# Optimization experiments

Hardware: AMD Instinct MI355X
Metric: run time of the kernel (lower is better)

## Reference

```python
import jax, jax.numpy as jnp
import numpy as np

WH, WW = 7, 7
N_TOK = WH * WW


def _buffers():
    # relative_coords_table: [1, 2*WH-1, 2*WW-1, 2], Swin-V2 log-spaced coords
    ch = np.arange(-(WH - 1), WH, dtype=np.float32)
    cw = np.arange(-(WW - 1), WW, dtype=np.float32)
    t = np.stack(np.meshgrid(ch, cw, indexing='ij'), axis=-1)[None]
    t[..., 0] /= (WH - 1)
    t[..., 1] /= (WW - 1)
    t *= 8.0
    t = np.sign(t) * np.log2(np.abs(t) + 1.0) / np.log2(8.0)
    # relative_position_index: [N, N]
    coords = np.stack(np.meshgrid(np.arange(WH), np.arange(WW), indexing='ij'))
    cf = coords.reshape(2, -1)
    rc = (cf[:, :, None] - cf[:, None, :]).transpose(1, 2, 0).astype(np.int32)
    rc[..., 0] += WH - 1
    rc[..., 1] += WW - 1
    rc[..., 0] *= 2 * WW - 1
    idx = rc.sum(-1)
    return jnp.asarray(t, jnp.float32), jnp.asarray(idx, jnp.int32)


def setup_inputs() -> dict:
    key = jax.random.key(0)
    ks = jax.random.split(key, 10)
    C, H = 384, 12
    B_, nW = 2048, 64
    rel_table, rel_index = _buffers()
    s = 0.02
    return {
        'x': jax.random.normal(ks[0], (B_, N_TOK, C), jnp.float32),
        'mask': jax.random.normal(ks[1], (nW, N_TOK, N_TOK), jnp.float32),
        'qkv_w': jax.random.normal(ks[2], (3 * C, C), jnp.float32) * s,
        'q_bias': jnp.zeros((C,), jnp.float32),
        'v_bias': jnp.zeros((C,), jnp.float32),
        'logit_scale': jnp.full((H, 1, 1), np.log(10.0), jnp.float32),
        'cpb_w1': jax.random.normal(ks[3], (512, 2), jnp.float32) * s,
        'cpb_b1': jnp.zeros((512,), jnp.float32),
        'cpb_w2': jax.random.normal(ks[4], (H, 512), jnp.float32) * s,
        'proj_w': jax.random.normal(ks[5], (C, C), jnp.float32) * s,
        'proj_b': jnp.zeros((C,), jnp.float32),
        'rel_table': rel_table,
        'rel_index': rel_index,
    }


def reference(x, mask, qkv_w, q_bias, v_bias, logit_scale, cpb_w1, cpb_b1,
              cpb_w2, proj_w, proj_b, rel_table, rel_index):
    B_, N, C = x.shape
    H = logit_scale.shape[0]
    Dh = C // H
    nW = mask.shape[0]
    # qkv projection with q/v bias, zero bias for k
    qkv_bias = jnp.concatenate([q_bias, jnp.zeros_like(v_bias), v_bias])
    qkv = x @ qkv_w.T + qkv_bias                       # [B, N, 3C]
    qkv = qkv.reshape(B_, N, 3, H, Dh).transpose(2, 0, 3, 1, 4)
    q, k, v = qkv[0], qkv[1], qkv[2]                    # [B, H, N, Dh]
    # per-head clamped logit scale
    ls = jnp.exp(jnp.minimum(logit_scale, np.log(1.0 / 0.01)))  # [H,1,1]
    # continuous relative position bias via small MLP
    tbl = jax.nn.relu(rel_table @ cpb_w1.T + cpb_b1) @ cpb_w2.T  # [1,13,13,H]
    tbl = tbl.reshape(-1, H)
    rpb = tbl[rel_index.reshape(-1)].reshape(N, N, H).transpose(2, 0, 1)
    rpb = 16.0 * jax.nn.sigmoid(rpb)                    # [H, N, N]
    # cosine attention (kernel uses norm + 1e-6 in denominator)
    qn = q / (jnp.sqrt(jnp.sum(q * q, -1, keepdims=True)) + 1e-6)
    kn = k / (jnp.sqrt(jnp.sum(k * k, -1, keepdims=True)) + 1e-6)
    attn = jnp.einsum('bhnd,bhmd->bhnm', qn, kn) * ls[None]
    attn = attn + rpb[None]
    # shift mask: window index w = batch_index % nW
    attn = attn.reshape(B_ // nW, nW, H, N, N) + mask[None, :, None]
    attn = attn.reshape(B_, H, N, N)
    # stable softmax with kernel's +1e-6 in denominator
    m = jnp.max(attn, -1, keepdims=True)
    e = jnp.exp(attn - m)
    p = e / (jnp.sum(e, -1, keepdims=True) + 1e-6)
    out = jnp.einsum('bhnm,bhmd->bhnd', p, v)           # [B, H, N, Dh]
    out = out.transpose(0, 2, 1, 3).reshape(B_, N, C)
    return out @ proj_w.T + proj_b
```

## Files before the change

### kernel.cpp

```cpp
#include <hip/hip_runtime.h>
#include <hip/hip_bf16.h>

typedef __attribute__((ext_vector_type(8))) short bf16x8;
typedef __attribute__((ext_vector_type(4))) float f32x4;
typedef __attribute__((ext_vector_type(16))) float f32x16;
typedef __attribute__((ext_vector_type(8))) unsigned short u16x8;
typedef unsigned short ushort_t;

#define DEVFN static __device__ __forceinline__

DEVFN ushort_t f2bf(float f) {
  unsigned int u = __builtin_bit_cast(unsigned int, f);
  u += 0x7FFFu + ((u >> 16) & 1u);
  return (ushort_t)(u >> 16);
}

DEVFN unsigned int cvtpk_bf16(float lo, float hi) {
  unsigned int r;
  asm("v_cvt_pk_bf16_f32 %0, %1, %2" : "=v"(r) : "v"(lo), "v"(hi));
  return r;
}

DEVFN void gload_lds16(const ushort_t* g, ushort_t* l) {
  __builtin_amdgcn_global_load_lds(
      (const __attribute__((address_space(1))) void*)g,
      (__attribute__((address_space(3))) void*)l, 16, 0, 0);
}

#define WAIT_VM(n) do { asm volatile("s_waitcnt vmcnt(" #n ")" ::: "memory"); \
                        __builtin_amdgcn_sched_barrier(0); } while (0)
#define WAIT_LGKM0 do { asm volatile("s_waitcnt lgkmcnt(0)" ::: "memory"); \
                        __builtin_amdgcn_sched_barrier(0); } while (0)
#define RAW_BAR __builtin_amdgcn_s_barrier()

DEVFN int xcd_swz(int bid, int nwg) {
  int q = nwg >> 3, r = nwg & 7;
  int xcd = bid & 7, u = bid >> 3;
  return (xcd < r ? xcd * (q + 1) : r * (q + 1) + (xcd - r) * q) + u;
}

__global__ void k_prep_w(const float* __restrict__ qkv_w, const float* __restrict__ proj_w,
                         const float* __restrict__ q_bias, const float* __restrict__ v_bias,
                         ushort_t* __restrict__ qkv_wb, ushort_t* __restrict__ proj_wb,
                         float* __restrict__ qkv_bias) {
  int gid = blockIdx.x * blockDim.x + threadIdx.x;
  int stride = gridDim.x * blockDim.x;
  for (int i = gid; i < 1152 * 384; i += stride) qkv_wb[i] = f2bf(qkv_w[i]);
  for (int i = gid; i < 384 * 384; i += stride) proj_wb[i] = f2bf(proj_w[i]);
  for (int i = gid; i < 1152; i += stride)
    qkv_bias[i] = (i < 384) ? q_bias[i] : ((i < 768) ? 0.f : v_bias[i - 768]);
}

__global__ void k_xb(const float* __restrict__ x, ushort_t* __restrict__ xb, long n4) {
  long gid = (long)blockIdx.x * blockDim.x + threadIdx.x;
  long stride = (long)gridDim.x * blockDim.x;
  for (long i = gid; i < n4; i += stride) {
    float4 v = reinterpret_cast<const float4*>(x)[i];
    unsigned long long pk = (unsigned long long)f2bf(v.x) |
                            ((unsigned long long)f2bf(v.y) << 16) |
                            ((unsigned long long)f2bf(v.z) << 32) |
                            ((unsigned long long)f2bf(v.w) << 48);
    reinterpret_cast<unsigned long long*>(xb)[i] = pk;
  }
}

__global__ void k_prep_cpb(const float* __restrict__ rel_table, const float* __restrict__ cpb_w1,
                           const float* __restrict__ cpb_b1, const float* __restrict__ cpb_w2,
                           const float* __restrict__ logit_scale,
                           float* __restrict__ tbl, float* __restrict__ ls) {
  int lane = threadIdx.x;
  if (blockIdx.x == 169) {
    if (lane < 12) ls[lane] = __expf(fminf(logit_scale[lane], 4.605170185988092f));
    return;
  }
  int row = blockIdx.x;
  float t0 = rel_table[row * 2 + 0], t1 = rel_table[row * 2 + 1];
  float acc[12];
#pragma unroll
  for (int h = 0; h < 12; h++) acc[h] = 0.f;
  for (int j = lane; j < 512; j += 64) {
    float hj = fmaxf(cpb_w1[j * 2] * t0 + cpb_w1[j * 2 + 1] * t1 + cpb_b1[j], 0.f);
#pragma unroll
    for (int h = 0; h < 12; h++) acc[h] += cpb_w2[h * 512 + j] * hj;
  }
#pragma unroll
  for (int h = 0; h < 12; h++) {
    float v = acc[h];
    v += __shfl_xor(v, 1);  v += __shfl_xor(v, 2);  v += __shfl_xor(v, 4);
    v += __shfl_xor(v, 8);  v += __shfl_xor(v, 16); v += __shfl_xor(v, 32);
    if (lane == 0) tbl[row * 12 + h] = v;
  }
}

__global__ void k_prep_comb(const float* __restrict__ tbl, const int* __restrict__ rel_index,
                            const float* __restrict__ mask, float* __restrict__ comb) {
  int gid = blockIdx.x * blockDim.x + threadIdx.x;
  if (gid >= 64 * 12 * 2401) return;
  int ij = gid % 2401;
  int h = (gid / 2401) % 12;
  int w = gid / (2401 * 12);
  float t = tbl[rel_index[ij] * 12 + h];
  comb[gid] = 16.f / (1.f + __expf(-t)) + mask[w * 2401 + ij];
}

__global__ void __launch_bounds__(256, 2) k_qkv(const ushort_t* __restrict__ xb,
                                                const ushort_t* __restrict__ wb,
                                                const float* __restrict__ bias,
                                                const float* __restrict__ lsb,
                                                ushort_t* __restrict__ qkvn, int nmb) {
  __shared__ __align__(16) ushort_t As[2][128][64];
  __shared__ __align__(16) ushort_t Bs[2][128][64];
  const int tid = threadIdx.x;
  const int lane = tid & 63, wid = tid >> 6;
  const int wm = wid >> 1, wn = wid & 1;
  const int l15 = lane & 15, g = lane >> 4;
  const int t = xcd_swz(blockIdx.x, nmb * 9);
  const int m0 = (t / 9) * 128, n0 = (t % 9) * 128;
  f32x4 acc[4][4] = {};

  const int rb_ = (wid << 3) + (lane >> 3);
  const int cg_ = (lane & 7) ^ (rb_ & 7);
  const size_t so_ = (size_t)rb_ * 384 + cg_ * 8;
  const int lo_ = wid * 512;
  const ushort_t* gA = xb + (size_t)m0 * 384 + so_;
  const ushort_t* gB = wb + (size_t)n0 * 384 + so_;

#define QKV_STAGE(buf, kk)                                                   \
  {                                                                          \
    _Pragma("unroll")                                                        \
    for (int it = 0; it < 4; it++) {                                         \
      gload_lds16(gA + (kk) * 64 + (size_t)it * 12288,                       \
                  &As[buf][0][0] + lo_ + it * 2048);                         \
      gload_lds16(gB + (kk) * 64 + (size_t)it * 12288,                       \
                  &Bs[buf][0][0] + lo_ + it * 2048);                         \
    }                                                                        \
  }

#define QKV_COMPUTE(buf)                                                     \
  {                                                                          \
    _Pragma("unroll")                                                        \
    for (int ks = 0; ks < 64; ks += 32) {                                    \
      const int cxor = (ks >> 3) + g;                                        \
      bf16x8 a[4], b[4];                                                     \
      _Pragma("unroll")                                                      \
      for (int mi = 0; mi < 4; mi++) {                                       \
        int row = wm * 64 + mi * 16 + l15;                                   \
        a[mi] = *reinterpret_cast<const bf16x8*>(                            \
            &As[buf][row][(cxor ^ (row & 7)) * 8]);                          \
      }                                                                      \
      _Pragma("unroll")                                                      \
      for (int ni = 0; ni < 4; ni++) {                                       \
        int row = wn * 64 + ni * 16 + l15;                                   \
        b[ni] = *reinterpret_cast<const bf16x8*>(                            \
            &Bs[buf][row][(cxor ^ (row & 7)) * 8]);                          \
      }                                                                      \
      _Pragma("unroll")                                                      \
      for (int mi = 0; mi < 4; mi++)                                         \
        _Pragma("unroll")                                                    \
        for (int ni = 0; ni < 4; ni++)                                       \
          acc[mi][ni] = __builtin_amdgcn_mfma_f32_16x16x32_bf16(             \
              a[mi], b[ni], acc[mi][ni], 0, 0, 0);                           \
    }                                                                        \
  }

  QKV_STAGE(0, 0);
  QKV_STAGE(1, 1);
  WAIT_VM(8); RAW_BAR;
  QKV_COMPUTE(0); WAIT_LGKM0; RAW_BAR;
  QKV_STAGE(0, 2); WAIT_VM(8); RAW_BAR;
  QKV_COMPUTE(1); WAIT_LGKM0; RAW_BAR;
  QKV_STAGE(1, 3); WAIT_VM(8); RAW_BAR;
  QKV_COMPUTE(0); WAIT_LGKM0; RAW_BAR;
  QKV_STAGE(0, 4); WAIT_VM(8); RAW_BAR;
  QKV_COMPUTE(1); WAIT_LGKM0; RAW_BAR;
  QKV_STAGE(1, 5); WAIT_VM(8); RAW_BAR;
  QKV_COMPUTE(0); WAIT_LGKM0; RAW_BAR;
  WAIT_VM(0); RAW_BAR;
  QKV_COMPUTE(1);
#undef QKV_STAGE
#undef QKV_COMPUTE

  const int colbase = n0 + wn * 64;
  const int which = colbase / 384;
  const float scl0 = (which == 0) ? lsb[(colbase >> 5)] : 1.f;
  const float scl1 = (which == 0) ? lsb[(colbase >> 5) + 1] : 1.f;
  float bs[4];
#pragma unroll
  for (int ni = 0; ni < 4; ni++) bs[ni] = bias[colbase + ni * 16 + l15];
#pragma unroll
  for (int mi = 0; mi < 4; mi++) {
#pragma unroll
    for (int r = 0; r < 4; r++) {
      float v[4];
#pragma unroll
      for (int ni = 0; ni < 4; ni++) v[ni] = acc[mi][ni][r] + bs[ni];
      if (which < 2) {
        float ss0 = v[0] * v[0] + v[1] * v[1];
        float ss1 = v[2] * v[2] + v[3] * v[3];
        ss0 += __shfl_xor(ss0, 1); ss1 += __shfl_xor(ss1, 1);
        ss0 += __shfl_xor(ss0, 2); ss1 += __shfl_xor(ss1, 2);
        ss0 += __shfl_xor(ss0, 4); ss1 += __shfl_xor(ss1, 4);
        ss0 += __shfl_xor(ss0, 8); ss1 += __shfl_xor(ss1, 8);
        float rn0 = scl0 / (sqrtf(ss0) + 1e-6f);
        float rn1 = scl1 / (sqrtf(ss1) + 1e-6f);
        v[0] *= rn0; v[1] *= rn0; v[2] *= rn1; v[3] *= rn1;
      }
      int row = m0 + wm * 64 + mi * 16 + g * 4 + r;
      size_t base = (size_t)row * 1152 + colbase + l15;
#pragma unroll
      for (int ni = 0; ni < 4; ni++) qkvn[base + ni * 16] = f2bf(v[ni]);
    }
  }
}

__global__ void __launch_bounds__(256, 4) k_attn(const ushort_t* __restrict__ qkvn,
                                                 const float* __restrict__ comb,
                                                 ushort_t* __restrict__ attn,
                                                 int win_base, int nk) {
  __shared__ float comb_s[2401];
  __shared__ __align__(16) ushort_t Vt[4][32][72];
  const int tid = threadIdx.x;
  const int lane = tid & 63, wv = tid >> 6;
  const int l31 = lane & 31, hi = lane >> 5;
  const int h = blockIdx.y;
  const int wloc = blockIdx.x & 63;
  const int k = (blockIdx.x >> 6) * 4 + wv;
  const bool active = k < nk;
  const int w_abs = (win_base + wloc) & 63;

  {
    const float* ct = comb + ((size_t)w_abs * 12 + h) * 2401;
    for (int i = tid; i < 2401; i += 256) comb_s[i] = ct[i];
  }

  const size_t rowbase = (size_t)(wloc + 64 * k) * 49;

  if (active) {
#pragma unroll
    for (int pass = 0; pass < 4; pass++) {
      int t = pass * 16 + (lane >> 2);
      int d0 = (lane & 3) * 8;
      u16x8 v = {};
      if (t < 49)
        v = *reinterpret_cast<const u16x8*>(&qkvn[(rowbase + t) * 1152 + 768 + h * 32 + d0]);
#pragma unroll
      for (int j = 0; j < 8; j++) Vt[wv][d0 + j][t] = v[j];
    }
  }
  __syncthreads();
  if (!active) return;

  bf16x8 qf[2][2], kf[2][2];
#pragma unroll
  for (int b = 0; b < 2; b++) {
    int t = b * 32 + l31; if (t > 48) t = 48;
    size_t rb = (rowbase + t) * 1152 + h * 32 + hi * 8;
#pragma unroll
    for (int ks = 0; ks < 2; ks++) {
      qf[b][ks] = *reinterpret_cast<const bf16x8*>(&qkvn[rb + ks * 16]);
      kf[b][ks] = *reinterpret_cast<const bf16x8*>(&qkvn[rb + 384 + ks * 16]);
    }
  }
  f32x16 S[2][2] = {};
#pragma unroll
  for (int a = 0; a < 2; a++)
#pragma unroll
    for (int b = 0; b < 2; b++) {
      S[a][b] = __builtin_amdgcn_mfma_f32_32x32x16_bf16(kf[a][0], qf[b][0], S[a][b], 0, 0, 0);
      S[a][b] = __builtin_amdgcn_mfma_f32_32x32x16_bf16(kf[a][1], qf[b][1], S[a][b], 0, 0, 0);
    }

#pragma unroll
  for (int b = 0; b < 2; b++) {
    const int qt = b * 32 + l31;
    const int qi = qt > 48 ? 48 : qt;
    const float* crow_p = &comb_s[qi * 49];
    float m = -3.0e38f;
#pragma unroll
    for (int a = 0; a < 2; a++)
#pragma unroll
      for (int r = 0; r < 16; r++) {
        int kt = a * 32 + (r & 3) + 8 * (r >> 2) + 4 * hi;
        float v = (kt < 49) ? (S[a][b][r] + crow_p[kt]) : -3.0e38f;
        S[a][b][r] = v;
        m = fmaxf(m, v);
      }
    m = fmaxf(m, __shfl_xor(m, 32));
    float s = 0.f;
#pragma unroll
    for (int a = 0; a < 2; a++)
#pragma unroll
      for (int r = 0; r < 16; r++) {
        float e = __expf(S[a][b][r] - m);
        S[a][b][r] = e;
        s += e;
      }
    s += __shfl_xor(s, 32);
    const float inv = 1.f / (s + 1e-6f);
    unsigned int pkk[2][4][2];
#pragma unroll
    for (int a = 0; a < 2; a++)
#pragma unroll
      for (int c = 0; c < 4; c++) {
        pkk[a][c][0] = cvtpk_bf16(S[a][b][c * 4 + 0] * inv, S[a][b][c * 4 + 1] * inv);
        pkk[a][c][1] = cvtpk_bf16(S[a][b][c * 4 + 2] * inv, S[a][b][c * 4 + 3] * inv);
      }
    f32x16 O = {};
#pragma unroll
    for (int a = 0; a < 2; a++)
#pragma unroll
      for (int ks = 0; ks < 2; ks++) {
        unsigned int s0 = hi ? pkk[a][2 * ks][0] : pkk[a][2 * ks + 1][0];
        unsigned int s1 = hi ? pkk[a][2 * ks][1] : pkk[a][2 * ks + 1][1];
        unsigned int r0 = __shfl_xor(s0, 32);
        unsigned int r1 = __shfl_xor(s1, 32);
        unsigned int w0 = hi ? r0 : pkk[a][2 * ks][0];
        unsigned int w1 = hi ? r1 : pkk[a][2 * ks][1];
        unsigned int w2 = hi ? pkk[a][2 * ks + 1][0] : r0;
        unsigned int w3 = hi ? pkk[a][2 * ks + 1][1] : r1;
        uint4 wq = {w0, w1, w2, w3};
        bf16x8 pa = __builtin_bit_cast(bf16x8, wq);
        bf16x8 vb = *reinterpret_cast<const bf16x8*>(&Vt[wv][l31][a * 32 + ks * 16 + hi * 8]);
        O = __builtin_amdgcn_mfma_f32_32x32x16_bf16(pa, vb, O, 0, 0, 0);
      }
#pragma unroll
    for (int r = 0; r < 16; r++) {
      int qrow = b * 32 + (r & 3) + 8 * (r >> 2) + 4 * hi;
      if (qrow < 49)
        attn[(rowbase + qrow) * 384 + h * 32 + l31] = f2bf(O[r]);
    }
  }
}

__global__ void __launch_bounds__(256, 2) k_proj(const ushort_t* __restrict__ a,
                                                 const ushort_t* __restrict__ wb,
                                                 const float* __restrict__ pbias,
                                                 float* __restrict__ out, int nmb) {
  __shared__ __align__(16) ushort_t As[2][128][64];
  __shared__ __align__(16) ushort_t Bs[2][128][64];
  const int tid = threadIdx.x;
  const int lane = tid & 63, wid = tid >> 6;
  const int wm = wid >> 1, wn = wid & 1;
  const int l15 = lane & 15, g = lane >> 4;
  const int t = xcd_swz(blockIdx.x, nmb * 3);
  const int m0 = (t / 3) * 128, n0 = (t % 3) * 128;
  f32x4 acc[4][4] = {};

  const int rb_ = (wid << 3) + (lane >> 3);
  const int cg_ = (lane & 7) ^ (rb_ & 7);
  const size_t so_ = (size_t)rb_ * 384 + cg_ * 8;
  const int lo_ = wid * 512;
  const ushort_t* gA = a + (size_t)m0 * 384 + so_;
  const ushort_t* gB = wb + (size_t)n0 * 384 + so_;

#define PRJ_STAGE(buf, kk)                                                   \
  {                                                                          \
    _Pragma("unroll")                                                        \
    for (int it = 0; it < 4; it++) {                                         \
      gload_lds16(gA + (kk) * 64 + (size_t)it * 12288,                       \
                  &As[buf][0][0] + lo_ + it * 2048);                         \
      gload_lds16(gB + (kk) * 64 + (size_t)it * 12288,                       \
                  &Bs[buf][0][0] + lo_ + it * 2048);                         \
    }                                                                        \
  }

#define PRJ_COMPUTE(buf)                                                     \
  {                                                                          \
    _Pragma("unroll")                                                        \
    for (int ks = 0; ks < 64; ks += 32) {                                    \
      const int cxor = (ks >> 3) + g;                                        \
      bf16x8 av[4], bv[4];                                                   \
      _Pragma("unroll")                                                      \
      for (int mi = 0; mi < 4; mi++) {                                       \
        int row = wm * 64 + mi * 16 + l15;                                   \
        av[mi] = *reinterpret_cast<const bf16x8*>(                           \
            &As[buf][row][(cxor ^ (row & 7)) * 8]);                          \
      }                                                                      \
      _Pragma("unroll")                                                      \
      for (int ni = 0; ni < 4; ni++) {                                       \
        int row = wn * 64 + ni * 16 + l15;                                   \
        bv[ni] = *reinterpret_cast<const bf16x8*>(                           \
            &Bs[buf][row][(cxor ^ (row & 7)) * 8]);                          \
      }                                                                      \
      _Pragma("unroll")                                                      \
      for (int mi = 0; mi < 4; mi++)                                         \
        _Pragma("unroll")                                                    \
        for (int ni = 0; ni < 4; ni++)                                       \
          acc[mi][ni] = __builtin_amdgcn_mfma_f32_16x16x32_bf16(             \
              av[mi], bv[ni], acc[mi][ni], 0, 0, 0);                         \
    }                                                                        \
  }

  PRJ_STAGE(0, 0);
  PRJ_STAGE(1, 1);
  WAIT_VM(8); RAW_BAR;
  PRJ_COMPUTE(0); WAIT_LGKM0; RAW_BAR;
  PRJ_STAGE(0, 2); WAIT_VM(8); RAW_BAR;
  PRJ_COMPUTE(1); WAIT_LGKM0; RAW_BAR;
  PRJ_STAGE(1, 3); WAIT_VM(8); RAW_BAR;
  PRJ_COMPUTE(0); WAIT_LGKM0; RAW_BAR;
  PRJ_STAGE(0, 4); WAIT_VM(8); RAW_BAR;
  PRJ_COMPUTE(1); WAIT_LGKM0; RAW_BAR;
  PRJ_STAGE(1, 5); WAIT_VM(8); RAW_BAR;
  PRJ_COMPUTE(0); WAIT_LGKM0; RAW_BAR;
  WAIT_VM(0); RAW_BAR;
  PRJ_COMPUTE(1);
#undef PRJ_STAGE
#undef PRJ_COMPUTE

  const int colbase = n0 + wn * 64;
  float bs[4];
#pragma unroll
  for (int ni = 0; ni < 4; ni++) bs[ni] = pbias[colbase + ni * 16 + l15];
#pragma unroll
  for (int mi = 0; mi < 4; mi++)
#pragma unroll
    for (int r = 0; r < 4; r++) {
      int row = m0 + wm * 64 + mi * 16 + g * 4 + r;
#pragma unroll
      for (int ni = 0; ni < 4; ni++)
        out[(size_t)row * 384 + colbase + ni * 16 + l15] = acc[mi][ni][r] + bs[ni];
    }
}

extern "C" void kernel_launch(void* const* d_in, const int* in_sizes, int n_in,
                              void* d_out, int out_size, void* d_ws, size_t ws_size,
                              hipStream_t stream) {
  const float* x        = (const float*)d_in[0];
  const float* mask     = (const float*)d_in[1];
  const float* qkv_w    = (const float*)d_in[2];
  const float* q_bias   = (const float*)d_in[3];
  const float* v_bias   = (const float*)d_in[4];
  const float* logit_sc = (const float*)d_in[5];
  const float* cpb_w1   = (const float*)d_in[6];
  const float* cpb_b1   = (const float*)d_in[7];
  const float* cpb_w2   = (const float*)d_in[8];
  const float* proj_w   = (const float*)d_in[9];
  const float* proj_b   = (const float*)d_in[10];
  const float* rel_tab  = (const float*)d_in[11];
  const int*   rel_idx  = (const int*)d_in[12];
  float* out = (float*)d_out;

  char* p = (char*)d_ws;
  auto carve = [&](size_t bytes) { char* r = p; p += (bytes + 255) & ~(size_t)255; return r; };
  ushort_t* qkv_wb  = (ushort_t*)carve(1152 * 384 * 2);
  ushort_t* proj_wb = (ushort_t*)carve(384 * 384 * 2);
  float* qkv_bias   = (float*)carve(1152 * 4);
  float* tbl        = (float*)carve(169 * 12 * 4);
  float* lsb        = (float*)carve(12 * 4);
  float* comb       = (float*)carve((size_t)64 * 12 * 2401 * 4);
  size_t fixed = (size_t)(p - (char*)d_ws);
  size_t avail = ws_size > fixed ? ws_size - fixed : 0;

  int nc = 1;
  while (nc < 16) {
    size_t per = ((size_t)(2048 / nc)) * 49 * (384 + 1152 + 384) * 2 + (1 << 20);
    if (per <= avail) break;
    nc *= 2;
  }
  const int nwin = 2048 / nc;
  const size_t Mc = (size_t)nwin * 49;
  ushort_t* xbuf  = (ushort_t*)carve(Mc * 384 * 2);
  ushort_t* qkvn  = (ushort_t*)carve(Mc * 1152 * 2);
  ushort_t* attnb = (ushort_t*)carve(Mc * 384 * 2);
  const int nmb = (int)(Mc / 128);
  const int nk = nwin >> 6;

  k_prep_w<<<dim3(512), dim3(256), 0, stream>>>(qkv_w, proj_w, q_bias, v_bias, qkv_wb, proj_wb, qkv_bias);
  k_prep_cpb<<<dim3(170), dim3(64), 0, stream>>>(rel_tab, cpb_w1, cpb_b1, cpb_w2, logit_sc, tbl, lsb);
  k_prep_comb<<<dim3((64 * 12 * 2401 + 255) / 256), dim3(256), 0, stream>>>(tbl, rel_idx, mask, comb);

  for (int c = 0; c < nc; c++) {
    size_t roff = (size_t)c * Mc;
    k_xb<<<dim3(2048), dim3(256), 0, stream>>>(x + roff * 384, xbuf, (long)(Mc * 384 / 4));
    k_qkv<<<dim3(nmb * 9), dim3(256), 0, stream>>>(xbuf, qkv_wb, qkv_bias, lsb, qkvn, nmb);
    k_attn<<<dim3(64 * ((nk + 3) / 4), 12), dim3(256), 0, stream>>>(qkvn, comb, attnb, c * nwin, nk);
    k_proj<<<dim3(nmb * 3), dim3(256), 0, stream>>>(attnb, proj_wb, proj_b, out + roff * 384, nmb);
  }
}
```

Before: 439.0 us.

## Load GEMM weight fragments directly to registers, single-buffer activations in LDS

In both the QKV and projection GEMMs, the weight (B) operand is now read straight from global memory into per-lane registers, double-buffered across K steps, instead of being staged through LDS. Activations still go to LDS, but with a single buffer and __syncthreads barriers in place of the explicit vmcnt/lgkmcnt double-buffered pipeline. The aim is to cut LDS footprint and LDS traffic for B, which may raise occupancy. The cost is uncoalesced, higher-latency global reads for B, more registers per thread, and less overlap between the activation loads and the MFMA work.

```diff
diff --git a/kernel.cpp b/kernel.cpp
--- a/kernel.cpp
+++ b/kernel.cpp
@@ -26,12 +26,6 @@
       (const __attribute__((address_space(1))) void*)g,
       (__attribute__((address_space(3))) void*)l, 16, 0, 0);
 }
-
-#define WAIT_VM(n) do { asm volatile("s_waitcnt vmcnt(" #n ")" ::: "memory"); \
-                        __builtin_amdgcn_sched_barrier(0); } while (0)
-#define WAIT_LGKM0 do { asm volatile("s_waitcnt lgkmcnt(0)" ::: "memory"); \
-                        __builtin_amdgcn_sched_barrier(0); } while (0)
-#define RAW_BAR __builtin_amdgcn_s_barrier()
 
 DEVFN int xcd_swz(int bid, int nwg) {
   int q = nwg >> 3, r = nwg & 7;
@@ -108,8 +102,7 @@
                                                 const float* __restrict__ bias,
                                                 const float* __restrict__ lsb,
                                                 ushort_t* __restrict__ qkvn, int nmb) {
-  __shared__ __align__(16) ushort_t As[2][128][64];
-  __shared__ __align__(16) ushort_t Bs[2][128][64];
+  __shared__ __align__(16) ushort_t As[128][64];
   const int tid = threadIdx.x;
   const int lane = tid & 63, wid = tid >> 6;
   const int wm = wid >> 1, wn = wid & 1;
@@ -123,62 +116,68 @@
   const size_t so_ = (size_t)rb_ * 384 + cg_ * 8;
   const int lo_ = wid * 512;
   const ushort_t* gA = xb + (size_t)m0 * 384 + so_;
-  const ushort_t* gB = wb + (size_t)n0 * 384 + so_;
-
-#define QKV_STAGE(buf, kk)                                                   \
-  {                                                                          \
-    _Pragma("unroll")                                                        \
-    for (int it = 0; it < 4; it++) {                                         \
+  const ushort_t* gBp = wb + (size_t)(n0 + wn * 64 + l15) * 384 + g * 8;
+
+  bf16x8 bA[4][2], bB[4][2];
+
+#define ASTAGE(kk)                                                           \
+  { _Pragma("unroll")                                                        \
+    for (int it = 0; it < 4; it++)                                           \
       gload_lds16(gA + (kk) * 64 + (size_t)it * 12288,                       \
-                  &As[buf][0][0] + lo_ + it * 2048);                         \
-      gload_lds16(gB + (kk) * 64 + (size_t)it * 12288,                       \
-                  &Bs[buf][0][0] + lo_ + it * 2048);                         \
-    }                                                                        \
-  }
-
-#define QKV_COMPUTE(buf)                                                     \
-  {                                                                          \
-    _Pragma("unroll")                                                        \
-    for (int ks = 0; ks < 64; ks += 32) {                                    \
-      const int cxor = (ks >> 3) + g;                                        \
-      bf16x8 a[4], b[4];                                                     \
+                  &As[0][0] + lo_ + it * 2048); }
+
+#define BLOADM(br, kk)                                                       \
+  { _Pragma("unroll")                                                        \
+    for (int ni = 0; ni < 4; ni++)                                           \
+      _Pragma("unroll")                                                      \
+      for (int ks = 0; ks < 2; ks++)                                         \
+        br[ni][ks] = *reinterpret_cast<const bf16x8*>(                       \
+            &gBp[(size_t)(ni * 16) * 384 + (kk) * 64 + ks * 32]); }
+
+#define GCOMP(br)                                                            \
+  { _Pragma("unroll")                                                        \
+    for (int ks = 0; ks < 2; ks++) {                                         \
+      bf16x8 a[4];                                                           \
       _Pragma("unroll")                                                      \
       for (int mi = 0; mi < 4; mi++) {                                       \
         int row = wm * 64 + mi * 16 + l15;                                   \
         a[mi] = *reinterpret_cast<const bf16x8*>(                            \
-            &As[buf][row][(cxor ^ (row & 7)) * 8]);                          \
-      }                                                                      \
-      _Pragma("unroll")                                                      \
-      for (int ni = 0; ni < 4; ni++) {                                       \
-        int row = wn * 64 + ni * 16 + l15;                                   \
-        b[ni] = *reinterpret_cast<const bf16x8*>(                            \
-            &Bs[buf][row][(cxor ^ (row & 7)) * 8]);                          \
+            &As[row][(((ks * 4 + g) ^ (row & 7))) * 8]);                     \
       }                                                                      \
       _Pragma("unroll")                                                      \
       for (int mi = 0; mi < 4; mi++)                                         \
         _Pragma("unroll")                                                    \
         for (int ni = 0; ni < 4; ni++)                                       \
           acc[mi][ni] = __builtin_amdgcn_mfma_f32_16x16x32_bf16(             \
-              a[mi], b[ni], acc[mi][ni], 0, 0, 0);                           \
-    }                                                                        \
-  }
-
-  QKV_STAGE(0, 0);
-  QKV_STAGE(1, 1);
-  WAIT_VM(8); RAW_BAR;
-  QKV_COMPUTE(0); WAIT_LGKM0; RAW_BAR;
-  QKV_STAGE(0, 2); WAIT_VM(8); RAW_BAR;
-  QKV_COMPUTE(1); WAIT_LGKM0; RAW_BAR;
-  QKV_STAGE(1, 3); WAIT_VM(8); RAW_BAR;
-  QKV_COMPUTE(0); WAIT_LGKM0; RAW_BAR;
-  QKV_STAGE(0, 4); WAIT_VM(8); RAW_BAR;
-  QKV_COMPUTE(1); WAIT_LGKM0; RAW_BAR;
-  QKV_STAGE(1, 5); WAIT_VM(8); RAW_BAR;
-  QKV_COMPUTE(0); WAIT_LGKM0; RAW_BAR;
-  WAIT_VM(0); RAW_BAR;
-  QKV_COMPUTE(1);
-#undef QKV_STAGE
-#undef QKV_COMPUTE
+              a[mi], br[ni][ks], acc[mi][ni], 0, 0, 0);                      \
+    } }
+
+  ASTAGE(0); BLOADM(bA, 0);
+  __syncthreads();
+  BLOADM(bB, 1); GCOMP(bA);
+  __syncthreads();
+  ASTAGE(1);
+  __syncthreads();
+  BLOADM(bA, 2); GCOMP(bB);
+  __syncthreads();
+  ASTAGE(2);
+  __syncthreads();
+  BLOADM(bB, 3); GCOMP(bA);
+  __syncthreads();
+  ASTAGE(3);
+  __syncthreads();
+  BLOADM(bA, 4); GCOMP(bB);
+  __syncthreads();
+  ASTAGE(4);
+  __syncthreads();
+  BLOADM(bB, 5); GCOMP(bA);
+  __syncthreads();
+  ASTAGE(5);
+  __syncthreads();
+  GCOMP(bB);
+#undef ASTAGE
+#undef BLOADM
+#undef GCOMP
 
   const int colbase = n0 + wn * 64;
   const int which = colbase / 384;
@@ -336,8 +335,7 @@
                                                  const ushort_t* __restrict__ wb,
                                                  const float* __restrict__ pbias,
                                                  float* __restrict__ out, int nmb) {
-  __shared__ __align__(16) ushort_t As[2][128][64];
-  __shared__ __align__(16) ushort_t Bs[2][128][64];
+  __shared__ __align__(16) ushort_t As[128][64];
   const int tid = threadIdx.x;
   const int lane = tid & 63, wid = tid >> 6;
   const int wm = wid >> 1, wn = wid & 1;
@@ -351,62 +349,68 @@
   const size_t so_ = (size_t)rb_ * 384 + cg_ * 8;
   const int lo_ = wid * 512;
   const ushort_t* gA = a + (size_t)m0 * 384 + so_;
-  const ushort_t* gB = wb + (size_t)n0 * 384 + so_;
-
-#define PRJ_STAGE(buf, kk)                                                   \
-  {                                                                          \
-    _Pragma("unroll")                                                        \
-    for (int it = 0; it < 4; it++) {                                         \
+  const ushort_t* gBp = wb + (size_t)(n0 + wn * 64 + l15) * 384 + g * 8;
+
+  bf16x8 bA[4][2], bB[4][2];
+
+#define ASTAGE(kk)                                                           \
+  { _Pragma("unroll")                                                        \
+    for (int it = 0; it < 4; it++)                                           \
       gload_lds16(gA + (kk) * 64 + (size_t)it * 12288,                       \
-                  &As[buf][0][0] + lo_ + it * 2048);                         \
-      gload_lds16(gB + (kk) * 64 + (size_t)it * 12288,                       \
-                  &Bs[buf][0][0] + lo_ + it * 2048);                         \
-    }                                                                        \
-  }
-
-#define PRJ_COMPUTE(buf)                                                     \
-  {                                                                          \
-    _Pragma("unroll")                                                        \
-    for (int ks = 0; ks < 64; ks += 32) {                                    \
-      const int cxor = (ks >> 3) + g;                                        \
-      bf16x8 av[4], bv[4];                                                   \
+                  &As[0][0] + lo_ + it * 2048); }
+
+#define BLOADM(br, kk)                                                       \
+  { _Pragma("unroll")                                                        \
+    for (int ni = 0; ni < 4; ni++)                                           \
+      _Pragma("unroll")                                                      \
+      for (int ks = 0; ks < 2; ks++)                                         \
+        br[ni][ks] = *reinterpret_cast<const bf16x8*>(                       \
+            &gBp[(size_t)(ni * 16) * 384 + (kk) * 64 + ks * 32]); }
+
+#define GCOMP(br)                                                            \
+  { _Pragma("unroll")                                                        \
+    for (int ks = 0; ks < 2; ks++) {                                         \
+      bf16x8 av[4];                                                          \
       _Pragma("unroll")                                                      \
       for (int mi = 0; mi < 4; mi++) {                                       \
         int row = wm * 64 + mi * 16 + l15;                                   \
         av[mi] = *reinterpret_cast<const bf16x8*>(                           \
-            &As[buf][row][(cxor ^ (row & 7)) * 8]);                          \
-      }                                                                      \
-      _Pragma("unroll")                                                      \
-      for (int ni = 0; ni < 4; ni++) {                                       \
-        int row = wn * 64 + ni * 16 + l15;                                   \
-        bv[ni] = *reinterpret_cast<const bf16x8*>(                           \
-            &Bs[buf][row][(cxor ^ (row & 7)) * 8]);                          \
+            &As[row][(((ks * 4 + g) ^ (row & 7))) * 8]);                     \
       }                                                                      \
       _Pragma("unroll")                                                      \
       for (int mi = 0; mi < 4; mi++)                                         \
         _Pragma("unroll")                                                    \
         for (int ni = 0; ni < 4; ni++)                                       \
           acc[mi][ni] = __builtin_amdgcn_mfma_f32_16x16x32_bf16(             \
-              av[mi], bv[ni], acc[mi][ni], 0, 0, 0);                         \
-    }                                                                        \
-  }
-
-  PRJ_STAGE(0, 0);
-  PRJ_STAGE(1, 1);
-  WAIT_VM(8); RAW_BAR;
-  PRJ_COMPUTE(0); WAIT_LGKM0; RAW_BAR;
-  PRJ_STAGE(0, 2); WAIT_VM(8); RAW_BAR;
-  PRJ_COMPUTE(1); WAIT_LGKM0; RAW_BAR;
-  PRJ_STAGE(1, 3); WAIT_VM(8); RAW_BAR;
-  PRJ_COMPUTE(0); WAIT_LGKM0; RAW_BAR;
-  PRJ_STAGE(0, 4); WAIT_VM(8); RAW_BAR;
-  PRJ_COMPUTE(1); WAIT_LGKM0; RAW_BAR;
-  PRJ_STAGE(1, 5); WAIT_VM(8); RAW_BAR;
-  PRJ_COMPUTE(0); WAIT_LGKM0; RAW_BAR;
-  WAIT_VM(0); RAW_BAR;
-  PRJ_COMPUTE(1);
-#undef PRJ_STAGE
-#undef PRJ_COMPUTE
+              av[mi], br[ni][ks], acc[mi][ni], 0, 0, 0);                     \
+    } }
+
+  ASTAGE(0); BLOADM(bA, 0);
+  __syncthreads();
+  BLOADM(bB, 1); GCOMP(bA);
+  __syncthreads();
+  ASTAGE(1);
+  __syncthreads();
+  BLOADM(bA, 2); GCOMP(bB);
+  __syncthreads();
+  ASTAGE(2);
+  __syncthreads();
+  BLOADM(bB, 3); GCOMP(bA);
+  __syncthreads();
+  ASTAGE(3);
+  __syncthreads();
+  BLOADM(bA, 4); GCOMP(bB);
+  __syncthreads();
+  ASTAGE(4);
+  __syncthreads();
+  BLOADM(bB, 5); GCOMP(bA);
+  __syncthreads();
+  ASTAGE(5);
+  __syncthreads();
+  GCOMP(bB);
+#undef ASTAGE
+#undef BLOADM
+#undef GCOMP
 
   const int colbase = n0 + wn * 64;
   float bs[4];
```

After: 481.5 us. +9.7%, slower.
